# Optimization experiments

Measured on AMD Instinct MI355X. Metric: run time of the kernel, lower is better.

The kernel has to match this reference:

```python
import jax, jax.numpy as jnp
import numpy as np

B, D_IN, LAT, C = 16384, 512, 64, 8
HID = [1024, 512, 256]

def _lin(k, fi, fo, scale=0.02):
    k1, k2 = jax.random.split(k)
    return jax.random.normal(k1, (fi, fo), jnp.float32) * scale, jax.random.normal(k2, (fo,), jnp.float32) * scale

def _lin_c(k, fi, fo, scale=0.02):
    k1, k2 = jax.random.split(k)
    return jax.random.normal(k1, (C, fi, fo), jnp.float32) * scale, jax.random.normal(k2, (C, fo), jnp.float32) * scale

def setup_inputs() -> dict:
    key = jax.random.key(0)
    ks = jax.random.split(key, 16)
    x = jax.random.normal(ks[0], (B, D_IN), jnp.float32)
    cluster_labels = jax.random.randint(ks[1], (B,), 0, C, jnp.int32)
    eps = jax.random.normal(ks[2], (B, LAT), jnp.float32)
    # encoder: shared(512->1024), unshared(1024->512), shared(512->256)
    enc_W0, enc_b0 = _lin(ks[3], D_IN, HID[0])
    enc_Wu, enc_bu = _lin_c(ks[4], HID[0], HID[1])
    enc_W2, enc_b2 = _lin(ks[5], HID[1], HID[2])
    # shared latent heads
    mu_W, mu_b = _lin(ks[6], HID[2], LAT)
    lv_W, lv_b = _lin(ks[7], HID[2], LAT)
    # decoder (hidden_dims reversed = [256,512,1024]): unshared(64->256), shared(256->512), unshared(512->1024)
    dec_Wu0, dec_bu0 = _lin_c(ks[8], LAT, HID[2])
    dec_W1, dec_b1 = _lin(ks[9], HID[2], HID[1])
    dec_Wu2, dec_bu2 = _lin_c(ks[10], HID[1], HID[0])
    # per-cluster final layer (1024 -> input_dim), no activation (all-continuous)
    fin_W, fin_b = _lin_c(ks[11], HID[0], D_IN)
    return dict(x=x, cluster_labels=cluster_labels, eps=eps,
                enc_W0=enc_W0, enc_b0=enc_b0, enc_Wu=enc_Wu, enc_bu=enc_bu,
                enc_W2=enc_W2, enc_b2=enc_b2, mu_W=mu_W, mu_b=mu_b,
                lv_W=lv_W, lv_b=lv_b, dec_Wu0=dec_Wu0, dec_bu0=dec_bu0,
                dec_W1=dec_W1, dec_b1=dec_b1, dec_Wu2=dec_Wu2, dec_bu2=dec_bu2,
                fin_W=fin_W, fin_b=fin_b)

def _unshared(h, W, b, labels):
    # per-cluster GEMM then row-wise combine (mask-based dispatch, no row reorder)
    y = jnp.einsum('bi,cio->bco', h, W) + b[None]  # [B, C, out]
    return jnp.take_along_axis(y, labels[:, None, None], axis=1)[:, 0, :]

def reference(x, cluster_labels, eps,
              enc_W0, enc_b0, enc_Wu, enc_bu, enc_W2, enc_b2,
              mu_W, mu_b, lv_W, lv_b,
              dec_Wu0, dec_bu0, dec_W1, dec_b1, dec_Wu2, dec_bu2,
              fin_W, fin_b):
    lbl = cluster_labels.astype(jnp.int32)
    # encoder
    h = jax.nn.relu(x @ enc_W0 + enc_b0)
    h = jax.nn.relu(_unshared(h, enc_Wu, enc_bu, lbl))
    h = jax.nn.relu(h @ enc_W2 + enc_b2)
    mu = h @ mu_W + mu_b
    logvar = h @ lv_W + lv_b
    # reparameterize
    z = mu + jnp.exp(0.5 * logvar) * eps
    # decoder
    h = jax.nn.relu(_unshared(z, dec_Wu0, dec_bu0, lbl))
    h = jax.nn.relu(h @ dec_W1 + dec_b1)
    h = jax.nn.relu(_unshared(h, dec_Wu2, dec_bu2, lbl))
    # per-cluster final output layer (identity activation: all-continuous)
    recon = _unshared(h, fin_W, fin_b, lbl)
    return recon
```

## Files before the change

kernel.cpp:

```cpp
#include <hip/hip_runtime.h>

typedef _Float16 f16;
typedef __attribute__((ext_vector_type(8))) _Float16 f16x8;
typedef __attribute__((ext_vector_type(4))) _Float16 f16x4;
typedef __attribute__((ext_vector_type(4))) float    f32x4;

#define B_ROWS 16384
#define MPAD   17408
#define MTILES 136
#define NBLK   64

typedef __attribute__((address_space(1))) void as1_void;
typedef __attribute__((address_space(3))) void as3_void;

__device__ __forceinline__ void gl_lds16(const void* g, void* l) {
    __builtin_amdgcn_global_load_lds((const as1_void*)g, (as3_void*)l, 16, 0, 0);
}


__global__ __launch_bounds__(256) void k_init(int* rowmap, f16* zerobuf) {
    int i = blockIdx.x * 256 + threadIdx.x;
    if (i < MPAD) rowmap[i] = -1;
    if (i < 16) zerobuf[i] = (f16)0.f;
}

__global__ __launch_bounds__(256) void k_hist(const int* __restrict__ lbl, int* __restrict__ blockhist) {
    __shared__ int h[8];
    if (threadIdx.x < 8) h[threadIdx.x] = 0;
    __syncthreads();
    int i = blockIdx.x * 256 + threadIdx.x;
    atomicAdd(&h[lbl[i]], 1);
    __syncthreads();
    if (threadIdx.x < 8) blockhist[blockIdx.x * 8 + threadIdx.x] = h[threadIdx.x];
}

__global__ void k_offsets(const int* __restrict__ blockhist, int* offs, int* tilec, int* blockbase) {
    __shared__ int tot[8];
    __shared__ int so[9];
    int t = threadIdx.x;
    if (t < 8) {
        int s = 0;
        for (int b = 0; b < NBLK; ++b) s += blockhist[b * 8 + t];
        tot[t] = s;
    }
    __syncthreads();
    if (t == 0) {
        int o = 0;
        for (int c = 0; c < 8; ++c) { so[c] = o; o += (tot[c] + 127) & ~127; }
        so[8] = o;
        for (int c = 0; c < 9; ++c) offs[c] = so[c];
    }
    __syncthreads();
    if (t < 8) {
        int run = so[t];
        for (int b = 0; b < NBLK; ++b) {
            blockbase[b * 8 + t] = run;
            run += blockhist[b * 8 + t];
        }
    }
    if (t < MTILES) {
        int row = t * 128, c = 7;
        for (int cc = 0; cc < 8; ++cc)
            if (row >= so[cc] && row < so[cc + 1]) c = cc;
        tilec[t] = c;
    }
}

__global__ __launch_bounds__(256) void k_scatter(const int* __restrict__ lbl,
                                                 const int* __restrict__ blockbase,
                                                 int* __restrict__ rowmap) {
    __shared__ int cur[8];
    if (threadIdx.x < 8) cur[threadIdx.x] = blockbase[blockIdx.x * 8 + threadIdx.x];
    __syncthreads();
    int i = blockIdx.x * 256 + threadIdx.x;
    int c = lbl[i];
    int pos = atomicAdd(&cur[c], 1);
    rowmap[pos] = i;
}

__global__ __launch_bounds__(256) void k_cvt(const float* __restrict__ s, f16* __restrict__ d, int n4) {
    int i = blockIdx.x * 256 + threadIdx.x;
    if (i < n4) {
        float4 v = ((const float4*)s)[i];
        f16x4 o = {(f16)v.x, (f16)v.y, (f16)v.z, (f16)v.w};
        ((f16x4*)d)[i] = o;
    }
}

__global__ __launch_bounds__(256) void tq_k(const float* __restrict__ src, f16* __restrict__ dst,
                                            int K, int N, long srcCS, long dstCS) {
    __shared__ float t[32][33];
    src += (size_t)blockIdx.z * srcCS;
    dst += (size_t)blockIdx.z * dstCS;
    int n0 = blockIdx.x * 32, k0 = blockIdx.y * 32;
    int tx = threadIdx.x & 31, ty = threadIdx.x >> 5;
    #pragma unroll
    for (int i = 0; i < 32; i += 8)
        t[ty + i][tx] = src[(size_t)(k0 + ty + i) * N + n0 + tx];
    __syncthreads();
    #pragma unroll
    for (int i = 0; i < 32; i += 8)
        dst[(size_t)(n0 + ty + i) * K + k0 + tx] = (f16)t[tx][ty + i];
}

__global__ void k_biasz(const float* __restrict__ mb_, const float* __restrict__ lb_, float* bz) {
    int i = threadIdx.x;
    if (i < 64) bz[i] = mb_[i];
    else if (i < 128) bz[i] = lb_[i - 64];
}

__global__ __launch_bounds__(256) void k_reparam(const f16* __restrict__ muv, const float* __restrict__ eps,
                                                 const int* __restrict__ rowmap, f16* __restrict__ z) {
    int i = blockIdx.x * 256 + threadIdx.x;
    int p = i >> 6, j = i & 63;
    int g = rowmap[p];
    float e  = (g >= 0) ? eps[(size_t)g * 64 + j] : 0.f;
    float mu = (float)muv[(size_t)p * 128 + j];
    float lv = (float)muv[(size_t)p * 128 + 64 + j];
    z[i] = (f16)(mu + expf(0.5f * lv) * e);
}


template<int GATHER, int PERW, int RELU, int SCATTER>
__global__ __launch_bounds__(256) void gemm_k(
    const f16* __restrict__ A, const f16* __restrict__ Wt,
    const float* __restrict__ bias, f16* __restrict__ Out, float* __restrict__ OutF,
    const int* __restrict__ rowmap, const int* __restrict__ tilec,
    const f16* __restrict__ zerobuf, int K, int N)
{
    __shared__ __align__(16) f16 lA[128 * 32];
    __shared__ __align__(16) f16 lB[128 * 32];
    const int tid  = threadIdx.x;
    const int wave = tid >> 6;
    const int lane = tid & 63;
    const int tm = blockIdx.x, tn = blockIdx.y;
    const int r0 = tm * 128, n0 = tn * 128;

    const f16* wb = Wt;
    const float* bb = bias;
    if (PERW) {
        int c = tilec[tm];
        wb += (size_t)c * K * N;
        bb += (size_t)c * N;
    }

    const int srow = tid >> 2;
    const int skk  = (tid & 3) * 8;
    const f16 *pa0, *pa1;
    int stepA0 = 32, stepA1 = 32;
    if (GATHER) {
        int g0 = rowmap[r0 + srow];
        int g1 = rowmap[r0 + 64 + srow];
        pa0 = (g0 >= 0) ? (A + (size_t)g0 * K + skk) : zerobuf;
        pa1 = (g1 >= 0) ? (A + (size_t)g1 * K + skk) : zerobuf;
        if (g0 < 0) stepA0 = 0;
        if (g1 < 0) stepA1 = 0;
    } else {
        pa0 = A + (size_t)(r0 + srow) * K + skk;
        pa1 = A + (size_t)(r0 + 64 + srow) * K + skk;
    }
    const f16* pb0 = wb + (size_t)(n0 + srow) * K + skk;
    const f16* pb1 = wb + (size_t)(n0 + 64 + srow) * K + skk;

    char* lAw = (char*)lA + wave * 1024;
    char* lBw = (char*)lB + wave * 1024;

    const int mb = (wave >> 1) * 64;
    const int nb = (wave & 1) * 64;
    const int quad = lane >> 4;
    const int r16  = lane & 15;

    f32x4 acc[4][4];
    #pragma unroll
    for (int i = 0; i < 4; ++i)
        #pragma unroll
        for (int j = 0; j < 4; ++j)
            acc[i][j] = (f32x4){0.f, 0.f, 0.f, 0.f};

    const int nk = K >> 5;
    for (int kb = 0; kb < nk; ++kb) {
        gl_lds16(pa0, lAw);
        gl_lds16(pa1, lAw + 4096);
        gl_lds16(pb0, lBw);
        gl_lds16(pb1, lBw + 4096);
        __syncthreads();
        f16x8 af[4], bf[4];
        #pragma unroll
        for (int i = 0; i < 4; ++i)
            af[i] = *(const f16x8*)(lA + (mb + i * 16 + r16) * 32 + quad * 8);
        #pragma unroll
        for (int j = 0; j < 4; ++j)
            bf[j] = *(const f16x8*)(lB + (nb + j * 16 + r16) * 32 + quad * 8);
        #pragma unroll
        for (int i = 0; i < 4; ++i)
            #pragma unroll
            for (int j = 0; j < 4; ++j)
                acc[i][j] = __builtin_amdgcn_mfma_f32_16x16x32_f16(af[i], bf[j], acc[i][j], 0, 0, 0);
        __syncthreads();
        pa0 += stepA0; pa1 += stepA1; pb0 += 32; pb1 += 32;
    }

    float bv[4];
    #pragma unroll
    for (int j = 0; j < 4; ++j) bv[j] = bb[n0 + nb + j * 16 + r16];

    #pragma unroll
    for (int i = 0; i < 4; ++i) {
        #pragma unroll
        for (int r = 0; r < 4; ++r) {
            int orow = r0 + mb + i * 16 + quad * 4 + r;
            int g = 0;
            if (SCATTER) g = rowmap[orow];
            #pragma unroll
            for (int j = 0; j < 4; ++j) {
                int ocol = n0 + nb + j * 16 + r16;
                float v = acc[i][j][r] + bv[j];
                if (RELU) v = fmaxf(v, 0.f);
                if (SCATTER) {
                    if (g >= 0) OutF[(size_t)g * N + ocol] = v;
                } else {
                    Out[(size_t)orow * N + ocol] = (f16)v;
                }
            }
        }
    }
}


extern "C" void kernel_launch(void* const* d_in, const int* in_sizes, int n_in,
                              void* d_out, int out_size, void* d_ws, size_t ws_size,
                              hipStream_t stream) {
    const float* x      = (const float*)d_in[0];
    const int*   lbl    = (const int*)  d_in[1];
    const float* eps    = (const float*)d_in[2];
    const float* enc_W0 = (const float*)d_in[3];
    const float* enc_b0 = (const float*)d_in[4];
    const float* enc_Wu = (const float*)d_in[5];
    const float* enc_bu = (const float*)d_in[6];
    const float* enc_W2 = (const float*)d_in[7];
    const float* enc_b2 = (const float*)d_in[8];
    const float* mu_W   = (const float*)d_in[9];
    const float* mu_b   = (const float*)d_in[10];
    const float* lv_W   = (const float*)d_in[11];
    const float* lv_b   = (const float*)d_in[12];
    const float* dWu0   = (const float*)d_in[13];
    const float* dbu0   = (const float*)d_in[14];
    const float* dW1    = (const float*)d_in[15];
    const float* db1    = (const float*)d_in[16];
    const float* dWu2   = (const float*)d_in[17];
    const float* dbu2   = (const float*)d_in[18];
    const float* finW   = (const float*)d_in[19];
    const float* finb   = (const float*)d_in[20];
    float* out = (float*)d_out;
    (void)in_sizes; (void)n_in; (void)out_size; (void)ws_size;

    char* base = (char*)d_ws;
    size_t off = 0;
    auto alloc = [&](size_t bytes) { char* r = base + off; off = (off + bytes + 255) & ~(size_t)255; return r; };
    f16* xh     = (f16*)alloc((size_t)B_ROWS * 512 * 2);
    f16* buf1   = (f16*)alloc((size_t)MPAD * 1024 * 2);
    f16* buf2   = (f16*)alloc((size_t)MPAD * 512 * 2);
    f16* buf3   = (f16*)alloc((size_t)MPAD * 256 * 2);
    f16* muv    = (f16*)alloc((size_t)MPAD * 128 * 2);
    f16* zb     = (f16*)alloc((size_t)MPAD * 64 * 2);
    f16* w0t    = (f16*)alloc(1024ul * 512 * 2);
    f16* wut    = (f16*)alloc(8ul * 512 * 1024 * 2);
    f16* w2t    = (f16*)alloc(256ul * 512 * 2);
    f16* wzt    = (f16*)alloc(128ul * 256 * 2);
    f16* wd0t   = (f16*)alloc(8ul * 256 * 64 * 2);
    f16* wd1t   = (f16*)alloc(512ul * 256 * 2);
    f16* wd2t   = (f16*)alloc(8ul * 1024 * 512 * 2);
    f16* wft    = (f16*)alloc(8ul * 512 * 1024 * 2);
    float* bz   = (float*)alloc(128 * 4);
    int* rowmap = (int*)alloc(MPAD * 4);
    int* blockhist = (int*)alloc(NBLK * 8 * 4);
    int* blockbase = (int*)alloc(NBLK * 8 * 4);
    int* offs   = (int*)alloc(64);
    int* tilec  = (int*)alloc(MTILES * 4);
    f16* zerob  = (f16*)alloc(64);

    k_init<<<(MPAD + 255) / 256, 256, 0, stream>>>(rowmap, zerob);
    k_hist<<<NBLK, 256, 0, stream>>>(lbl, blockhist);
    k_offsets<<<1, 256, 0, stream>>>(blockhist, offs, tilec, blockbase);
    k_scatter<<<NBLK, 256, 0, stream>>>(lbl, blockbase, rowmap);
    k_cvt<<<(B_ROWS * 512 / 4 + 255) / 256, 256, 0, stream>>>(x, xh, B_ROWS * 512 / 4);
    k_biasz<<<1, 128, 0, stream>>>(mu_b, lv_b, bz);

    tq_k<<<dim3(32, 16, 1), 256, 0, stream>>>(enc_W0, w0t, 512, 1024, 0, 0);
    tq_k<<<dim3(16, 32, 8), 256, 0, stream>>>(enc_Wu, wut, 1024, 512, 1024l * 512, 512l * 1024);
    tq_k<<<dim3(8, 16, 1), 256, 0, stream>>>(enc_W2, w2t, 512, 256, 0, 0);
    tq_k<<<dim3(2, 8, 1), 256, 0, stream>>>(mu_W, wzt, 256, 64, 0, 0);
    tq_k<<<dim3(2, 8, 1), 256, 0, stream>>>(lv_W, wzt + 64 * 256, 256, 64, 0, 0);
    tq_k<<<dim3(8, 2, 8), 256, 0, stream>>>(dWu0, wd0t, 64, 256, 64l * 256, 256l * 64);
    tq_k<<<dim3(16, 8, 1), 256, 0, stream>>>(dW1, wd1t, 256, 512, 0, 0);
    tq_k<<<dim3(32, 16, 8), 256, 0, stream>>>(dWu2, wd2t, 512, 1024, 512l * 1024, 1024l * 512);
    tq_k<<<dim3(16, 32, 8), 256, 0, stream>>>(finW, wft, 1024, 512, 1024l * 512, 512l * 1024);

    gemm_k<1,0,1,0><<<dim3(MTILES, 8), 256, 0, stream>>>(xh,   w0t,  enc_b0, buf1, nullptr, rowmap, tilec, zerob, 512, 1024);
    gemm_k<0,1,1,0><<<dim3(MTILES, 4), 256, 0, stream>>>(buf1, wut,  enc_bu, buf2, nullptr, rowmap, tilec, zerob, 1024, 512);
    gemm_k<0,0,1,0><<<dim3(MTILES, 2), 256, 0, stream>>>(buf2, w2t,  enc_b2, buf3, nullptr, rowmap, tilec, zerob, 512, 256);
    gemm_k<0,0,0,0><<<dim3(MTILES, 1), 256, 0, stream>>>(buf3, wzt,  bz,     muv,  nullptr, rowmap, tilec, zerob, 256, 128);
    k_reparam<<<MPAD * 64 / 256, 256, 0, stream>>>(muv, eps, rowmap, zb);
    gemm_k<0,1,1,0><<<dim3(MTILES, 2), 256, 0, stream>>>(zb,   wd0t, dbu0,   buf3, nullptr, rowmap, tilec, zerob, 64, 256);
    gemm_k<0,0,1,0><<<dim3(MTILES, 4), 256, 0, stream>>>(buf3, wd1t, db1,    buf2, nullptr, rowmap, tilec, zerob, 256, 512);
    gemm_k<0,1,1,0><<<dim3(MTILES, 8), 256, 0, stream>>>(buf2, wd2t, dbu2,   buf1, nullptr, rowmap, tilec, zerob, 512, 1024);
    gemm_k<0,1,0,1><<<dim3(MTILES, 4), 256, 0, stream>>>(buf1, wft,  finb,   nullptr, out,  rowmap, tilec, zerob, 1024, 512);
}
```

Before: 395.6 us.

## Fuse prep and transpose launches, deepen GEMM K-tile with swizzled LDS, remap blocks per XCD

Four setup kernels are merged into one, and the input conversion plus nine weight transposes run as a single segmented launch, cutting launch overhead. The GEMM K-step doubles from 32 to 64 and uses an XOR swizzle on LDS addresses to avoid bank conflicts. Blocks are remapped on a 1D grid so consecutive M tiles land on the same XCD for better L2 reuse. LDS use doubles and the mapping assumes MTILES=136 (17*8).

```diff
diff --git a/kernel.cpp b/kernel.cpp
--- a/kernel.cpp
+++ b/kernel.cpp
@@ -18,20 +18,25 @@
 }
 
 
-__global__ __launch_bounds__(256) void k_init(int* rowmap, f16* zerobuf) {
-    int i = blockIdx.x * 256 + threadIdx.x;
-    if (i < MPAD) rowmap[i] = -1;
-    if (i < 16) zerobuf[i] = (f16)0.f;
-}
-
-__global__ __launch_bounds__(256) void k_hist(const int* __restrict__ lbl, int* __restrict__ blockhist) {
-    __shared__ int h[8];
-    if (threadIdx.x < 8) h[threadIdx.x] = 0;
-    __syncthreads();
-    int i = blockIdx.x * 256 + threadIdx.x;
-    atomicAdd(&h[lbl[i]], 1);
-    __syncthreads();
-    if (threadIdx.x < 8) blockhist[blockIdx.x * 8 + threadIdx.x] = h[threadIdx.x];
+__global__ __launch_bounds__(256) void k_prep(const int* __restrict__ lbl, int* __restrict__ blockhist,
+                                              int* __restrict__ rowmap,
+                                              const float* __restrict__ mb_, const float* __restrict__ lb_,
+                                              float* __restrict__ bz, f16* __restrict__ zerob) {
+    int b = blockIdx.x, t = threadIdx.x;
+    int i = b * 256 + t;
+    rowmap[i] = -1;
+    if (b < NBLK) {
+        __shared__ int h[8];
+        if (t < 8) h[t] = 0;
+        __syncthreads();
+        atomicAdd(&h[lbl[i]], 1);
+        __syncthreads();
+        if (t < 8) blockhist[b * 8 + t] = h[t];
+    } else if (b == NBLK) {
+        if (t < 64) zerob[t] = (f16)0.f;
+        if (t < 64) bz[t] = mb_[t];
+        else if (t < 128) bz[t] = lb_[t - 64];
+    }
 }
 
 __global__ void k_offsets(const int* __restrict__ blockhist, int* offs, int* tilec, int* blockbase) {
@@ -78,35 +83,38 @@
     rowmap[pos] = i;
 }
 
-__global__ __launch_bounds__(256) void k_cvt(const float* __restrict__ s, f16* __restrict__ d, int n4) {
-    int i = blockIdx.x * 256 + threadIdx.x;
-    if (i < n4) {
-        float4 v = ((const float4*)s)[i];
+
+struct Seg { const float* s; f16* d; int K, N, b0, nx, ny; long sCS, dCS; };
+struct SegTab { Seg g[10]; };
+
+__global__ __launch_bounds__(256) void k_trans(SegTab tab, const float* __restrict__ x, f16* __restrict__ xh) {
+    int bid = blockIdx.x;
+    if (bid < tab.g[1].b0) {
+        int i = bid * 256 + threadIdx.x;
+        float4 v = ((const float4*)x)[i];
         f16x4 o = {(f16)v.x, (f16)v.y, (f16)v.z, (f16)v.w};
-        ((f16x4*)d)[i] = o;
-    }
-}
-
-__global__ __launch_bounds__(256) void tq_k(const float* __restrict__ src, f16* __restrict__ dst,
-                                            int K, int N, long srcCS, long dstCS) {
+        ((f16x4*)xh)[i] = o;
+        return;
+    }
+    int s = 9;
+    while (bid < tab.g[s].b0) --s;
+    Seg sg = tab.g[s];
+    int lb = bid - sg.b0;
+    int nxy = sg.nx * sg.ny;
+    int z = lb / nxy; int r = lb - z * nxy;
+    int by = r / sg.nx; int bx = r - by * sg.nx;
+    const float* src = sg.s + (size_t)z * sg.sCS;
+    f16* dst = sg.d + (size_t)z * sg.dCS;
+    int n0 = bx * 32, k0 = by * 32;
+    int tx = threadIdx.x & 31, ty = threadIdx.x >> 5;
     __shared__ float t[32][33];
-    src += (size_t)blockIdx.z * srcCS;
-    dst += (size_t)blockIdx.z * dstCS;
-    int n0 = blockIdx.x * 32, k0 = blockIdx.y * 32;
-    int tx = threadIdx.x & 31, ty = threadIdx.x >> 5;
     #pragma unroll
     for (int i = 0; i < 32; i += 8)
-        t[ty + i][tx] = src[(size_t)(k0 + ty + i) * N + n0 + tx];
+        t[ty + i][tx] = src[(size_t)(k0 + ty + i) * sg.N + n0 + tx];
     __syncthreads();
     #pragma unroll
     for (int i = 0; i < 32; i += 8)
-        dst[(size_t)(n0 + ty + i) * K + k0 + tx] = (f16)t[tx][ty + i];
-}
-
-__global__ void k_biasz(const float* __restrict__ mb_, const float* __restrict__ lb_, float* bz) {
-    int i = threadIdx.x;
-    if (i < 64) bz[i] = mb_[i];
-    else if (i < 128) bz[i] = lb_[i - 64];
+        dst[(size_t)(n0 + ty + i) * sg.K + k0 + tx] = (f16)t[tx][ty + i];
 }
 
 __global__ __launch_bounds__(256) void k_reparam(const f16* __restrict__ muv, const float* __restrict__ eps,
@@ -128,12 +136,17 @@
     const int* __restrict__ rowmap, const int* __restrict__ tilec,
     const f16* __restrict__ zerobuf, int K, int N)
 {
-    __shared__ __align__(16) f16 lA[128 * 32];
-    __shared__ __align__(16) f16 lB[128 * 32];
+    __shared__ __align__(16) f16 lA[128 * 64];
+    __shared__ __align__(16) f16 lB[128 * 64];
     const int tid  = threadIdx.x;
     const int wave = tid >> 6;
     const int lane = tid & 63;
-    const int tm = blockIdx.x, tn = blockIdx.y;
+
+    const int id  = blockIdx.x;
+    const int xcd = id & 7;
+    const int jj  = id >> 3;
+    const int tm  = (jj % 17) * 8 + xcd;
+    const int tn  = jj / 17;
     const int r0 = tm * 128, n0 = tn * 128;
 
     const f16* wb = Wt;
@@ -144,31 +157,31 @@
         bb += (size_t)c * N;
     }
 
-    const int srow = tid >> 2;
-    const int skk  = (tid & 3) * 8;
-    const f16 *pa0, *pa1;
-    int stepA0 = 32, stepA1 = 32;
-    if (GATHER) {
-        int g0 = rowmap[r0 + srow];
-        int g1 = rowmap[r0 + 64 + srow];
-        pa0 = (g0 >= 0) ? (A + (size_t)g0 * K + skk) : zerobuf;
-        pa1 = (g1 >= 0) ? (A + (size_t)g1 * K + skk) : zerobuf;
-        if (g0 < 0) stepA0 = 0;
-        if (g1 < 0) stepA1 = 0;
-    } else {
-        pa0 = A + (size_t)(r0 + srow) * K + skk;
-        pa1 = A + (size_t)(r0 + 64 + srow) * K + skk;
-    }
-    const f16* pb0 = wb + (size_t)(n0 + srow) * K + skk;
-    const f16* pb1 = wb + (size_t)(n0 + 64 + srow) * K + skk;
-
-    char* lAw = (char*)lA + wave * 1024;
-    char* lBw = (char*)lB + wave * 1024;
+    const int srow = tid >> 3;
+    const int sg   = tid & 7;
+    const int xk16 = (sg ^ (srow & 7)) * 16;
+    const size_t rowB = (size_t)K * 2;
+    const size_t passB = 32 * rowB;
+
+    const char* pa[4]; size_t stepA[4];
+    #pragma unroll
+    for (int p = 0; p < 4; ++p) {
+        int gr = r0 + p * 32 + srow;
+        if (GATHER) {
+            int g = rowmap[gr];
+            if (g >= 0) { pa[p] = (const char*)(A + (size_t)g * K) + xk16; stepA[p] = 128; }
+            else        { pa[p] = (const char*)zerobuf;                    stepA[p] = 0;   }
+        } else {
+            pa[p] = (const char*)(A + (size_t)gr * K) + xk16; stepA[p] = 128;
+        }
+    }
+    const char* pb = (const char*)(wb + (size_t)(n0 + srow) * K) + xk16;
 
     const int mb = (wave >> 1) * 64;
     const int nb = (wave & 1) * 64;
     const int quad = lane >> 4;
     const int r16  = lane & 15;
+    const int key  = r16 & 7;
 
     f32x4 acc[4][4];
     #pragma unroll
@@ -177,27 +190,35 @@
         for (int j = 0; j < 4; ++j)
             acc[i][j] = (f32x4){0.f, 0.f, 0.f, 0.f};
 
-    const int nk = K >> 5;
+    const int nk = K >> 6;
     for (int kb = 0; kb < nk; ++kb) {
-        gl_lds16(pa0, lAw);
-        gl_lds16(pa1, lAw + 4096);
-        gl_lds16(pb0, lBw);
-        gl_lds16(pb1, lBw + 4096);
+        #pragma unroll
+        for (int p = 0; p < 4; ++p)
+            gl_lds16(pa[p], (char*)lA + p * 4096 + wave * 1024);
+        #pragma unroll
+        for (int p = 0; p < 4; ++p)
+            gl_lds16(pb + p * passB, (char*)lB + p * 4096 + wave * 1024);
         __syncthreads();
-        f16x8 af[4], bf[4];
-        #pragma unroll
-        for (int i = 0; i < 4; ++i)
-            af[i] = *(const f16x8*)(lA + (mb + i * 16 + r16) * 32 + quad * 8);
-        #pragma unroll
-        for (int j = 0; j < 4; ++j)
-            bf[j] = *(const f16x8*)(lB + (nb + j * 16 + r16) * 32 + quad * 8);
-        #pragma unroll
-        for (int i = 0; i < 4; ++i)
+        #pragma unroll
+        for (int kk = 0; kk < 2; ++kk) {
+            const int off = ((kk * 4 + quad) ^ key) * 16;
+            f16x8 af[4], bf[4];
+            #pragma unroll
+            for (int i = 0; i < 4; ++i)
+                af[i] = *(const f16x8*)((const char*)lA + (mb + i * 16 + r16) * 128 + off);
             #pragma unroll
             for (int j = 0; j < 4; ++j)
-                acc[i][j] = __builtin_amdgcn_mfma_f32_16x16x32_f16(af[i], bf[j], acc[i][j], 0, 0, 0);
+                bf[j] = *(const f16x8*)((const char*)lB + (nb + j * 16 + r16) * 128 + off);
+            #pragma unroll
+            for (int i = 0; i < 4; ++i)
+                #pragma unroll
+                for (int j = 0; j < 4; ++j)
+                    acc[i][j] = __builtin_amdgcn_mfma_f32_16x16x32_f16(af[i], bf[j], acc[i][j], 0, 0, 0);
+        }
         __syncthreads();
-        pa0 += stepA0; pa1 += stepA1; pb0 += 32; pb1 += 32;
+        #pragma unroll
+        for (int p = 0; p < 4; ++p) pa[p] += stepA[p];
+        pb += 128;
     }
 
     float bv[4];
@@ -277,32 +298,38 @@
     int* blockbase = (int*)alloc(NBLK * 8 * 4);
     int* offs   = (int*)alloc(64);
     int* tilec  = (int*)alloc(MTILES * 4);
-    f16* zerob  = (f16*)alloc(64);
-
-    k_init<<<(MPAD + 255) / 256, 256, 0, stream>>>(rowmap, zerob);
-    k_hist<<<NBLK, 256, 0, stream>>>(lbl, blockhist);
+    f16* zerob  = (f16*)alloc(256);
+
+    k_prep<<<MPAD / 256, 256, 0, stream>>>(lbl, blockhist, rowmap, mu_b, lv_b, bz, zerob);
     k_offsets<<<1, 256, 0, stream>>>(blockhist, offs, tilec, blockbase);
     k_scatter<<<NBLK, 256, 0, stream>>>(lbl, blockbase, rowmap);
-    k_cvt<<<(B_ROWS * 512 / 4 + 255) / 256, 256, 0, stream>>>(x, xh, B_ROWS * 512 / 4);
-    k_biasz<<<1, 128, 0, stream>>>(mu_b, lv_b, bz);
-
-    tq_k<<<dim3(32, 16, 1), 256, 0, stream>>>(enc_W0, w0t, 512, 1024, 0, 0);
-    tq_k<<<dim3(16, 32, 8), 256, 0, stream>>>(enc_Wu, wut, 1024, 512, 1024l * 512, 512l * 1024);
-    tq_k<<<dim3(8, 16, 1), 256, 0, stream>>>(enc_W2, w2t, 512, 256, 0, 0);
-    tq_k<<<dim3(2, 8, 1), 256, 0, stream>>>(mu_W, wzt, 256, 64, 0, 0);
-    tq_k<<<dim3(2, 8, 1), 256, 0, stream>>>(lv_W, wzt + 64 * 256, 256, 64, 0, 0);
-    tq_k<<<dim3(8, 2, 8), 256, 0, stream>>>(dWu0, wd0t, 64, 256, 64l * 256, 256l * 64);
-    tq_k<<<dim3(16, 8, 1), 256, 0, stream>>>(dW1, wd1t, 256, 512, 0, 0);
-    tq_k<<<dim3(32, 16, 8), 256, 0, stream>>>(dWu2, wd2t, 512, 1024, 512l * 1024, 1024l * 512);
-    tq_k<<<dim3(16, 32, 8), 256, 0, stream>>>(finW, wft, 1024, 512, 1024l * 512, 512l * 1024);
-
-    gemm_k<1,0,1,0><<<dim3(MTILES, 8), 256, 0, stream>>>(xh,   w0t,  enc_b0, buf1, nullptr, rowmap, tilec, zerob, 512, 1024);
-    gemm_k<0,1,1,0><<<dim3(MTILES, 4), 256, 0, stream>>>(buf1, wut,  enc_bu, buf2, nullptr, rowmap, tilec, zerob, 1024, 512);
-    gemm_k<0,0,1,0><<<dim3(MTILES, 2), 256, 0, stream>>>(buf2, w2t,  enc_b2, buf3, nullptr, rowmap, tilec, zerob, 512, 256);
-    gemm_k<0,0,0,0><<<dim3(MTILES, 1), 256, 0, stream>>>(buf3, wzt,  bz,     muv,  nullptr, rowmap, tilec, zerob, 256, 128);
+
+    SegTab tab;
+    int b0 = B_ROWS * 512 / 4 / 256;
+    auto seg = [&](int i, const float* s, f16* d, int K, int N, int nz, long sCS, long dCS) {
+        int nx = N / 32, ny = K / 32;
+        tab.g[i] = Seg{s, d, K, N, b0, nx, ny, sCS, dCS};
+        b0 += nx * ny * nz;
+    };
+    tab.g[0] = Seg{nullptr, nullptr, 0, 0, 0, 0, 0, 0, 0};
+    seg(1, enc_W0, w0t, 512, 1024, 1, 0, 0);
+    seg(2, enc_Wu, wut, 1024, 512, 8, 1024l * 512, 512l * 1024);
+    seg(3, enc_W2, w2t, 512, 256, 1, 0, 0);
+    seg(4, mu_W, wzt, 256, 64, 1, 0, 0);
+    seg(5, lv_W, wzt + 64 * 256, 256, 64, 1, 0, 0);
+    seg(6, dWu0, wd0t, 64, 256, 8, 64l * 256, 256l * 64);
+    seg(7, dW1, wd1t, 256, 512, 1, 0, 0);
+    seg(8, dWu2, wd2t, 512, 1024, 8, 512l * 1024, 1024l * 512);
+    seg(9, finW, wft, 1024, 512, 8, 1024l * 512, 512l * 1024);
+    k_trans<<<b0, 256, 0, stream>>>(tab, x, xh);
+
+    gemm_k<1,0,1,0><<<MTILES * 8, 256, 0, stream>>>(xh,   w0t,  enc_b0, buf1, nullptr, rowmap, tilec, zerob, 512, 1024);
+    gemm_k<0,1,1,0><<<MTILES * 4, 256, 0, stream>>>(buf1, wut,  enc_bu, buf2, nullptr, rowmap, tilec, zerob, 1024, 512);
+    gemm_k<0,0,1,0><<<MTILES * 2, 256, 0, stream>>>(buf2, w2t,  enc_b2, buf3, nullptr, rowmap, tilec, zerob, 512, 256);
+    gemm_k<0,0,0,0><<<MTILES * 1, 256, 0, stream>>>(buf3, wzt,  bz,     muv,  nullptr, rowmap, tilec, zerob, 256, 128);
     k_reparam<<<MPAD * 64 / 256, 256, 0, stream>>>(muv, eps, rowmap, zb);
-    gemm_k<0,1,1,0><<<dim3(MTILES, 2), 256, 0, stream>>>(zb,   wd0t, dbu0,   buf3, nullptr, rowmap, tilec, zerob, 64, 256);
-    gemm_k<0,0,1,0><<<dim3(MTILES, 4), 256, 0, stream>>>(buf3, wd1t, db1,    buf2, nullptr, rowmap, tilec, zerob, 256, 512);
-    gemm_k<0,1,1,0><<<dim3(MTILES, 8), 256, 0, stream>>>(buf2, wd2t, dbu2,   buf1, nullptr, rowmap, tilec, zerob, 512, 1024);
-    gemm_k<0,1,0,1><<<dim3(MTILES, 4), 256, 0, stream>>>(buf1, wft,  finb,   nullptr, out,  rowmap, tilec, zerob, 1024, 512);
-}
+    gemm_k<0,1,1,0><<<MTILES * 2, 256, 0, stream>>>(zb,   wd0t, dbu0,   buf3, nullptr, rowmap, tilec, zerob, 64, 256);
+    gemm_k<0,0,1,0><<<MTILES * 4, 256, 0, stream>>>(buf3, wd1t, db1,    buf2, nullptr, rowmap, tilec, zerob, 256, 512);
+    gemm_k<0,1,1,0><<<MTILES * 8, 256, 0, stream>>>(buf2, wd2t, dbu2,   buf1, nullptr, rowmap, tilec, zerob, 512, 1024);
+    gemm_k<0,1,0,1><<<MTILES * 4, 256, 0, stream>>>(buf1, wft,  finb,   nullptr, out,  rowmap, tilec, zerob, 1024, 512);
+}
```

Result: faster. 362.3 us (-8.4%).
